# Kernel optimization log

Measured on AMD Instinct MI355X. Metric: run time of the kernel, lower is better.

The kernel has to match this reference:

```python
import jax, jax.numpy as jnp
import numpy as np

DT = 0.01
REG = 0.01

def setup_inputs() -> dict:
    key = jax.random.key(0)
    k1, k2, k3, k4 = jax.random.split(key, 4)
    B, C_in, L = 16, 128, 4096
    C_out, KS = 256, 9
    return {
        "x": jax.random.normal(k1, (B, C_in, L), dtype=jnp.float32),
        "weight": jax.random.normal(k2, (C_out, C_in, KS), dtype=jnp.float32) * np.sqrt(2.0 / (C_out * KS)),
        "bias": jnp.zeros((C_out,), dtype=jnp.float32),
        "vel": jax.random.normal(k3, (C_in, KS), dtype=jnp.float32) * 0.1,
        "acc": jax.random.normal(k4, (C_in, KS), dtype=jnp.float32) * 0.01,
        "ks": 9,
        "stride": 1,
        "pad": 4,
    }

def reference(x, weight, bias, vel, acc, ks, stride, pad):
    # x: [B, C_in, L]
    if pad > 0:
        x = jnp.pad(x, ((0, 0), (0, 0), (pad, pad)), mode="edge")  # replicate pad
    L_pad = x.shape[2]
    L_out = (L_pad - ks) // stride + 1
    t_off = jnp.arange(ks, dtype=jnp.float32) * DT  # [ks]
    # unfold: gather sliding windows -> [B, C_in, L_out, ks]
    idx = jnp.arange(L_out)[:, None] * stride + jnp.arange(ks)[None, :]
    xu = x[:, :, idx]
    # per-tap physics offset: vel*t + 0.5*acc*t^2, shape [C_in, ks] broadcast
    offset = vel * t_off + 0.5 * acc * (t_off ** 2)  # [C_in, ks]
    xt = xu + offset[None, :, None, :]  # [B, C_in, L_out, ks]
    # GEMM: [B, L_out, C_in*ks] x [C_in*ks, C_out]
    out = jnp.einsum("bclk,ock->bol", xt, weight) + bias[None, :, None]
    phys = REG * (jnp.mean(vel ** 2) + jnp.mean(acc ** 2))
    return (out, phys)
```

## Files before the change

### kernel.cpp

```cpp
#include <hip/hip_runtime.h>
#include <hip/hip_bf16.h>

typedef unsigned short u16;
typedef __bf16 bf16x8 __attribute__((ext_vector_type(8)));
typedef float f32x4 __attribute__((ext_vector_type(4)));
typedef unsigned short ushort8 __attribute__((ext_vector_type(8)));

#define C_IN   128
#define C_OUT  256
#define BATCH  16
#define LEN    4096
#define KS     9
#define PAD    4
#define LPAD   (LEN + 2*PAD)
#define KTOT   (C_IN * KS)
#define NSTEP  36

__device__ inline u16 f2bf(float f) {
    __hip_bfloat16 h = __float2bfloat16(f);
    return __builtin_bit_cast(u16, h);
}

__device__ __forceinline__ void g2l16(const void* g, void* l) {
    __builtin_amdgcn_global_load_lds(
        (const __attribute__((address_space(1))) void*)g,
        (__attribute__((address_space(3))) void*)l, 16, 0, 0);
}

__global__ void prep_xt(const float* __restrict__ x, u16* __restrict__ xt) {
    int b    = blockIdx.y;
    int lane = threadIdx.x & 63;
    int jb   = threadIdx.x >> 6;
    int lp   = blockIdx.x * 64 + lane;
    if (lp >= LPAD) return;
    int l = lp - PAD;
    l = l < 0 ? 0 : (l > LEN - 1 ? LEN - 1 : l);
    const float* xb = x + (size_t)b * C_IN * LEN + l;
    u16* row = xt + ((size_t)b * LPAD + lp) * C_IN;
    int key = lp & 7;
    #pragma unroll
    for (int jj = 0; jj < 4; ++jj) {
        int cblk = jb * 4 + jj;
        ushort8 v;
        #pragma unroll
        for (int e = 0; e < 8; ++e)
            v[e] = f2bf(xb[(size_t)(cblk * 8 + e) * LEN]);
        int jstore = cblk ^ key;
        *reinterpret_cast<ushort8*>(row + jstore * 8) = v;
    }
}

__global__ void prep_w3(const float* __restrict__ w, u16* __restrict__ w3) {
    int i = blockIdx.x * 256 + threadIdx.x;
    if (i >= C_OUT * KTOT) return;
    int e  = i & 7;
    int r  = i >> 3;
    int kg = r & 3;
    int mr = (r >> 2) & 15;
    int ob = (r >> 6) & 15;
    int s  = r >> 10;
    int o  = ob * 16 + mr;
    int k  = s >> 2;
    int c  = (s & 3) * 32 + kg * 8 + e;
    w3[i] = f2bf(w[((size_t)o * C_IN + c) * KS + k]);
}

__global__ void prep_ebias(const float* __restrict__ w, const float* __restrict__ bias,
                           const float* __restrict__ vel, const float* __restrict__ acc,
                           float* __restrict__ ebias, float* __restrict__ phys_out) {
    __shared__ float red[256];
    int o = blockIdx.x;
    int t = threadIdx.x;
    float sum = 0.f;
    for (int i = t; i < KTOT; i += 256) {
        int k = i % KS;
        float tk = k * 0.01f;
        float off = vel[i] * tk + 0.5f * acc[i] * tk * tk;
        sum += off * w[(size_t)o * KTOT + i];
    }
    red[t] = sum;
    __syncthreads();
    for (int h = 128; h > 0; h >>= 1) {
        if (t < h) red[t] += red[t + h];
        __syncthreads();
    }
    if (t == 0) ebias[o] = bias[o] + red[0];

    if (o == 0) {
        __syncthreads();
        float pv = 0.f;
        for (int i = t; i < KTOT; i += 256) {
            float v = vel[i], a = acc[i];
            pv += v * v + a * a;
        }
        red[t] = pv;
        __syncthreads();
        for (int h = 128; h > 0; h >>= 1) {
            if (t < h) red[t] += red[t + h];
            __syncthreads();
        }
        if (t == 0) *phys_out = 0.01f * (red[0] / (float)KTOT);
    }
}

__global__ __launch_bounds__(256, 3) void conv_main(const u16* __restrict__ xt,
                                                    const u16* __restrict__ w3,
                                                    const float* __restrict__ ebias,
                                                    float* __restrict__ out) {
    __shared__ u16 ldsx[136 * 128];
    __shared__ u16 ldsa[2][4096];

    int b     = blockIdx.z;
    int obase = blockIdx.y * 128;
    int lbase = blockIdx.x * 128;
    int t     = threadIdx.x;
    int lane  = t & 63;
    int w     = t >> 6;
    int wm    = w >> 1;
    int wn    = w & 1;

    int mrow = lane & 15;
    int kgrp = lane >> 4;

    const u16* asrc = w3 + (size_t)(obase >> 4) * 512;

    {
        const u16* bsrc = xt + ((size_t)b * LPAD + lbase) * C_IN;
        #pragma unroll
        for (int j = 0; j < 8; ++j)
            g2l16(bsrc + (j * 256 + t) * 8, ldsx + (j * 256 + w * 64) * 8);
        if (t < 128)
            g2l16(bsrc + (2048 + t) * 8, ldsx + (2048 + w * 64) * 8);
        #pragma unroll
        for (int j = 0; j < 2; ++j)
            g2l16(asrc + (j * 256 + t) * 8, ldsa[0] + (j * 256 + w * 64) * 8);
    }
    __syncthreads();

    f32x4 acc[4][4] = {};
    const char* ldsbase = reinterpret_cast<const char*>(ldsx);
    int afoff = (wm << 12) + ((mrow * 4 + kgrp) << 4);

    #define LOAD_A_LDS(BUF, AF)                                                  \
        {                                                                        \
            const char* ab_ = reinterpret_cast<const char*>(ldsa[BUF]) + afoff;  \
            _Pragma("unroll")                                                    \
            for (int mi = 0; mi < 4; ++mi)                                       \
                AF[mi] = *reinterpret_cast<const bf16x8*>(ab_ + (mi << 10));     \
        }
    #define LOAD_B(S, BF)                                                        \
        {                                                                        \
            int k_ = (S) >> 2;                                                   \
            int coff_ = ((S) & 3) * 64 + kgrp * 16;                              \
            _Pragma("unroll")                                                    \
            for (int ni = 0; ni < 4; ++ni) {                                     \
                int row_  = wn * 64 + ni * 16 + mrow + k_;                       \
                int addr_ = row_ * 256 + coff_;                                  \
                addr_ ^= (row_ & 7) << 4;                                        \
                BF[ni] = *reinterpret_cast<const bf16x8*>(ldsbase + addr_);      \
            }                                                                    \
        }
    #define STAGE_A(S, BUF)                                                      \
        {                                                                        \
            const u16* as_ = asrc + (size_t)(S) * 8192;                          \
            _Pragma("unroll")                                                    \
            for (int j = 0; j < 2; ++j)                                          \
                g2l16(as_ + (j * 256 + t) * 8, ldsa[BUF] + (j * 256 + w * 64) * 8); \
        }
    #define MFMA16(AF, BF)                                                       \
        {                                                                        \
            _Pragma("unroll")                                                    \
            for (int ni = 0; ni < 4; ++ni)                                       \
                _Pragma("unroll")                                                \
                for (int mi = 0; mi < 4; ++mi)                                   \
                    acc[mi][ni] = __builtin_amdgcn_mfma_f32_16x16x32_bf16(       \
                        AF[mi], BF[ni], acc[mi][ni], 0, 0, 0);                   \
        }

    bf16x8 a0[4], a1[4], b0[4], b1[4];
    LOAD_A_LDS(0, a0);
    LOAD_B(0, b0);

    #pragma unroll 1
    for (int s = 0; s < NSTEP; s += 2) {
        if (s + 1 < NSTEP) STAGE_A(s + 1, 1);
        LOAD_B(s + 1, b1);
        MFMA16(a0, b0);
        __syncthreads();
        LOAD_A_LDS(1, a1);
        if (s + 2 < NSTEP) STAGE_A(s + 2, 0);
        LOAD_B(s + 2 < NSTEP ? s + 2 : 0, b0);
        MFMA16(a1, b1);
        __syncthreads();
        LOAD_A_LDS(0, a0);
    }

    #pragma unroll
    for (int mi = 0; mi < 4; ++mi) {
        int o0 = obase + wm * 64 + mi * 16 + kgrp * 4;
        f32x4 eb = *reinterpret_cast<const f32x4*>(ebias + o0);
        #pragma unroll
        for (int ni = 0; ni < 4; ++ni) {
            int l = lbase + wn * 64 + ni * 16 + mrow;
            float* op = out + (size_t)(b * C_OUT + o0) * LEN + l;
            #pragma unroll
            for (int r = 0; r < 4; ++r)
                op[(size_t)r * LEN] = acc[mi][ni][r] + eb[r];
        }
    }
    #undef LOAD_A_LDS
    #undef LOAD_B
    #undef STAGE_A
    #undef MFMA16
}

extern "C" void kernel_launch(void* const* d_in, const int* in_sizes, int n_in,
                              void* d_out, int out_size, void* d_ws, size_t ws_size,
                              hipStream_t stream) {
    const float* x      = (const float*)d_in[0];
    const float* weight = (const float*)d_in[1];
    const float* bias   = (const float*)d_in[2];
    const float* vel    = (const float*)d_in[3];
    const float* acc    = (const float*)d_in[4];
    float* out = (float*)d_out;

    char* ws = (char*)d_ws;
    u16*  xt    = (u16*)ws;
    u16*  w3    = (u16*)(ws + (size_t)BATCH * LPAD * C_IN * 2);
    float* ebias = (float*)(ws + (size_t)BATCH * LPAD * C_IN * 2 + (size_t)C_OUT * KTOT * 2);

    hipLaunchKernelGGL(prep_xt, dim3((LPAD + 63) / 64, BATCH), dim3(256), 0, stream, x, xt);
    hipLaunchKernelGGL(prep_w3, dim3((C_OUT * KTOT + 255) / 256), dim3(256), 0, stream, weight, w3);
    hipLaunchKernelGGL(prep_ebias, dim3(C_OUT), dim3(256), 0, stream,
                       weight, bias, vel, acc, ebias, out + (size_t)BATCH * C_OUT * LEN);
    hipLaunchKernelGGL(conv_main, dim3(LEN / 128, C_OUT / 128, BATCH), dim3(256), 0, stream,
                       xt, w3, ebias, out);
}
```

Measured before the change: 63.86 us.

## Deepen weight staging to four LDS buffers and widen swizzle, merge prep kernels

The main conv kernel now keeps four LDS buffers for weight tiles, prefetching three steps ahead. Waits use explicit vmcnt/lgkmcnt counters with one barrier per step instead of two syncthreads per pair of steps, and the K loop is fully unrolled. The xt swizzle key widens from 3 to 4 bits to reduce LDS bank conflicts, and the weight layout is reordered so A fragments load contiguously per lane. The weight-prep and bias-prep kernels are merged into one launch; occupancy hint drops from 3 to 2 blocks per CU because of the larger LDS footprint.

```diff
diff --git a/kernel.cpp b/kernel.cpp
--- a/kernel.cpp
+++ b/kernel.cpp
@@ -37,7 +37,7 @@
     l = l < 0 ? 0 : (l > LEN - 1 ? LEN - 1 : l);
     const float* xb = x + (size_t)b * C_IN * LEN + l;
     u16* row = xt + ((size_t)b * LPAD + lp) * C_IN;
-    int key = lp & 7;
+    int key = lp & 15;
     #pragma unroll
     for (int jj = 0; jj < 4; ++jj) {
         int cblk = jb * 4 + jj;
@@ -50,27 +50,27 @@
     }
 }
 
-__global__ void prep_w3(const float* __restrict__ w, u16* __restrict__ w3) {
-    int i = blockIdx.x * 256 + threadIdx.x;
-    if (i >= C_OUT * KTOT) return;
-    int e  = i & 7;
-    int r  = i >> 3;
-    int kg = r & 3;
-    int mr = (r >> 2) & 15;
-    int ob = (r >> 6) & 15;
-    int s  = r >> 10;
-    int o  = ob * 16 + mr;
-    int k  = s >> 2;
-    int c  = (s & 3) * 32 + kg * 8 + e;
-    w3[i] = f2bf(w[((size_t)o * C_IN + c) * KS + k]);
-}
-
-__global__ void prep_ebias(const float* __restrict__ w, const float* __restrict__ bias,
-                           const float* __restrict__ vel, const float* __restrict__ acc,
-                           float* __restrict__ ebias, float* __restrict__ phys_out) {
+__global__ void prep_wb(const float* __restrict__ w, const float* __restrict__ bias,
+                        const float* __restrict__ vel, const float* __restrict__ acc,
+                        u16* __restrict__ w4, float* __restrict__ ebias,
+                        float* __restrict__ phys_out) {
+    int t = threadIdx.x;
+    if (blockIdx.x < 1152) {
+        int i = blockIdx.x * 256 + t;
+        int e  = i & 7;
+        int r  = i >> 3;
+        int mr = r & 15;
+        int kg = (r >> 4) & 3;
+        int ob = (r >> 6) & 15;
+        int s  = r >> 10;
+        int o  = ob * 16 + mr;
+        int k  = s >> 2;
+        int c  = (s & 3) * 32 + kg * 8 + e;
+        w4[i] = f2bf(w[((size_t)o * C_IN + c) * KS + k]);
+        return;
+    }
     __shared__ float red[256];
-    int o = blockIdx.x;
-    int t = threadIdx.x;
+    int o = blockIdx.x - 1152;
     float sum = 0.f;
     for (int i = t; i < KTOT; i += 256) {
         int k = i % KS;
@@ -103,12 +103,12 @@
     }
 }
 
-__global__ __launch_bounds__(256, 3) void conv_main(const u16* __restrict__ xt,
-                                                    const u16* __restrict__ w3,
+__global__ __launch_bounds__(256, 2) void conv_main(const u16* __restrict__ xt,
+                                                    const u16* __restrict__ w4,
                                                     const float* __restrict__ ebias,
                                                     float* __restrict__ out) {
-    __shared__ u16 ldsx[136 * 128];
-    __shared__ u16 ldsa[2][4096];
+    __shared__ u16 ldsx[17408];
+    __shared__ u16 ldsa[4][4096];
 
     int b     = blockIdx.z;
     int obase = blockIdx.y * 128;
@@ -118,11 +118,10 @@
     int w     = t >> 6;
     int wm    = w >> 1;
     int wn    = w & 1;
-
-    int mrow = lane & 15;
-    int kgrp = lane >> 4;
-
-    const u16* asrc = w3 + (size_t)(obase >> 4) * 512;
+    int mrow  = lane & 15;
+    int kgrp  = lane >> 4;
+
+    const u16* asrc = w4 + (size_t)(obase >> 4) * 512;
 
     {
         const u16* bsrc = xt + ((size_t)b * LPAD + lbase) * C_IN;
@@ -132,16 +131,19 @@
         if (t < 128)
             g2l16(bsrc + (2048 + t) * 8, ldsx + (2048 + w * 64) * 8);
         #pragma unroll
-        for (int j = 0; j < 2; ++j)
-            g2l16(asrc + (j * 256 + t) * 8, ldsa[0] + (j * 256 + w * 64) * 8);
+        for (int p = 0; p < 3; ++p)
+            #pragma unroll
+            for (int j = 0; j < 2; ++j)
+                g2l16(asrc + (size_t)p * 8192 + (j * 256 + t) * 8,
+                      ldsa[p] + (j * 256 + w * 64) * 8);
     }
     __syncthreads();
 
     f32x4 acc[4][4] = {};
     const char* ldsbase = reinterpret_cast<const char*>(ldsx);
-    int afoff = (wm << 12) + ((mrow * 4 + kgrp) << 4);
-
-    #define LOAD_A_LDS(BUF, AF)                                                  \
+    int afoff = (wm << 12) + lane * 16;
+
+    #define LOAD_A_BUF(BUF, AF)                                                  \
         {                                                                        \
             const char* ab_ = reinterpret_cast<const char*>(ldsa[BUF]) + afoff;  \
             _Pragma("unroll")                                                    \
@@ -156,7 +158,7 @@
             for (int ni = 0; ni < 4; ++ni) {                                     \
                 int row_  = wn * 64 + ni * 16 + mrow + k_;                       \
                 int addr_ = row_ * 256 + coff_;                                  \
-                addr_ ^= (row_ & 7) << 4;                                        \
+                addr_ ^= (row_ & 15) << 4;                                       \
                 BF[ni] = *reinterpret_cast<const bf16x8*>(ldsbase + addr_);      \
             }                                                                    \
         }
@@ -177,22 +179,22 @@
                         AF[mi], BF[ni], acc[mi][ni], 0, 0, 0);                   \
         }
 
-    bf16x8 a0[4], a1[4], b0[4], b1[4];
-    LOAD_A_LDS(0, a0);
-    LOAD_B(0, b0);
-
-    #pragma unroll 1
-    for (int s = 0; s < NSTEP; s += 2) {
-        if (s + 1 < NSTEP) STAGE_A(s + 1, 1);
-        LOAD_B(s + 1, b1);
-        MFMA16(a0, b0);
-        __syncthreads();
-        LOAD_A_LDS(1, a1);
-        if (s + 2 < NSTEP) STAGE_A(s + 2, 0);
-        LOAD_B(s + 2 < NSTEP ? s + 2 : 0, b0);
-        MFMA16(a1, b1);
-        __syncthreads();
-        LOAD_A_LDS(0, a0);
+    bf16x8 ar[2][4], br[2][4];
+    LOAD_A_BUF(0, ar[0]);
+    LOAD_B(0, br[0]);
+
+    #pragma unroll
+    for (int s = 0; s < NSTEP; ++s) {
+        const int cur = s & 1, nx = cur ^ 1;
+        if (s + 3 < NSTEP) STAGE_A(s + 3, (s + 3) & 3);
+        if (s + 1 < NSTEP) { LOAD_A_BUF((s + 1) & 3, ar[nx]); LOAD_B(s + 1, br[nx]); }
+        MFMA16(ar[cur], br[cur]);
+        if (s + 1 < NSTEP) {
+            if (s + 3 < NSTEP) asm volatile("s_waitcnt vmcnt(2)" ::: "memory");
+            else               asm volatile("s_waitcnt vmcnt(0)" ::: "memory");
+            asm volatile("s_waitcnt lgkmcnt(0)" ::: "memory");
+            __builtin_amdgcn_s_barrier();
+        }
     }
 
     #pragma unroll
@@ -208,7 +210,7 @@
                 op[(size_t)r * LEN] = acc[mi][ni][r] + eb[r];
         }
     }
-    #undef LOAD_A_LDS
+    #undef LOAD_A_BUF
     #undef LOAD_B
     #undef STAGE_A
     #undef MFMA16
@@ -226,13 +228,12 @@
 
     char* ws = (char*)d_ws;
     u16*  xt    = (u16*)ws;
-    u16*  w3    = (u16*)(ws + (size_t)BATCH * LPAD * C_IN * 2);
+    u16*  w4    = (u16*)(ws + (size_t)BATCH * LPAD * C_IN * 2);
     float* ebias = (float*)(ws + (size_t)BATCH * LPAD * C_IN * 2 + (size_t)C_OUT * KTOT * 2);
 
     hipLaunchKernelGGL(prep_xt, dim3((LPAD + 63) / 64, BATCH), dim3(256), 0, stream, x, xt);
-    hipLaunchKernelGGL(prep_w3, dim3((C_OUT * KTOT + 255) / 256), dim3(256), 0, stream, weight, w3);
-    hipLaunchKernelGGL(prep_ebias, dim3(C_OUT), dim3(256), 0, stream,
-                       weight, bias, vel, acc, ebias, out + (size_t)BATCH * C_OUT * LEN);
+    hipLaunchKernelGGL(prep_wb, dim3(1152 + 256), dim3(256), 0, stream,
+                       weight, bias, vel, acc, w4, ebias, out + (size_t)BATCH * C_OUT * LEN);
     hipLaunchKernelGGL(conv_main, dim3(LEN / 128, C_OUT / 128, BATCH), dim3(256), 0, stream,
-                       xt, w3, ebias, out);
-}
+                       xt, w4, ebias, out);
+}
```

After: 61.30 us. 4.0% less time.
